# Kernel tuning notes

Measured on AMD Instinct MI355X. Metric: run time of the kernel, lower is better.

## Reference

```python
import jax, jax.numpy as jnp
import numpy as np

H_D, W_D = 64, 64          # 1024x1024 image / 16 patch size
N = H_D * W_D              # 4096 patches
D = 768                    # DINO ViT-B/16 embed dim
ALPHA = 0.5
K = 100


def setup_inputs() -> dict:
    key = jax.random.key(0)
    k1, k2 = jax.random.split(key)
    out = jax.random.normal(k1, (N, D), dtype=jnp.float32)
    attn_seed = jax.random.randint(k2, (2,), 0, H_D, dtype=jnp.int32)
    return {"out": out, "attn_seed": attn_seed}


def _connected_components(mask):
    """8-connectivity connected components via iterative min-label propagation.
    Background = 0. Foreground pixels get the minimum initial id (+1) of their
    component (same partition as cv2.connectedComponents, different numbering)."""
    fg = mask > 0
    BIG = jnp.int32(N + 1)
    init = jnp.where(fg, jnp.arange(N, dtype=jnp.int32).reshape(H_D, W_D) + 1, BIG)

    def step(l):
        p = jnp.pad(l, 1, constant_values=N + 1)
        m = l
        for dy in (0, 1, 2):          # fixed 3x3 neighborhood, not a data-dim loop
            for dx in (0, 1, 2):
                m = jnp.minimum(m, p[dy:dy + H_D, dx:dx + W_D])
        return jnp.where(fg, m, BIG)

    def cond(st):
        l, prev = st
        return jnp.any(l != prev)

    def body(st):
        l, _ = st
        return step(l), l

    l, _ = jax.lax.while_loop(cond, body, (step(init), init))
    return jnp.where(fg, l, 0)


def reference(out, attn_seed):
    # similarity between all patch features: [N, N]
    sim = out @ out.T
    deg = sim >= 0                                        # degree_matrix (bool)
    # patch with fewest non-negative similarities
    seed_degree_flat = jnp.argmin(deg.sum(axis=0)).astype(jnp.int32)
    seed_degree = jnp.stack([seed_degree_flat // W_D, seed_degree_flat % W_D])
    # blend degree seed with attention seed
    seed_rc = jnp.round(ALPHA * seed_degree + (1.0 - ALPHA) * attn_seed).astype(jnp.int32)
    seed = seed_rc[0] * W_D + seed_rc[1]

    # initial expansion set = patches positively correlated with the seed
    s = deg[seed].astype(jnp.int32)
    s = s.at[seed].set(1)                                 # degree_matrix[seed][seed] = 255 (truthy)
    order = jnp.argsort(-sim[seed])                       # descending
    s = s.at[order[K:]].set(0)                            # keep top-k most similar

    # sequential seed expansion (updates feed into later iterations)
    def step(s, i):
        grows = jnp.sum(sim[i] * (s == 1)) > 0
        s = s.at[i].set(jnp.where(s[i] == 0, 0, jnp.where(grows, 1, 0)))
        return s, None

    s, _ = jax.lax.scan(step, s, jnp.arange(N))

    return _connected_components(s.reshape(H_D, W_D))
```

## Files before the change

kernel.cpp:

```cpp
#include <hip/hip_runtime.h>
#include <cstdint>

#define NP   4096
#define DD   768
#define HD   64
#define WD   64
#define KTOP 100

typedef short bf16x8 __attribute__((ext_vector_type(8)));
typedef float f32x4  __attribute__((ext_vector_type(4)));

__device__ __forceinline__ void gload_lds16(const void* g, void* l) {
    __builtin_amdgcn_global_load_lds(
        (const __attribute__((address_space(1))) unsigned int*)(uintptr_t)g,
        (__attribute__((address_space(3))) unsigned int*)(unsigned int)(uintptr_t)l,
        16, 0, 0);
}

__device__ __forceinline__ unsigned short f2bf_rne(float x) {
    unsigned b = __float_as_uint(x);
    unsigned r = b + 0x7FFFu + ((b >> 16) & 1u);
    return (unsigned short)(r >> 16);
}
__device__ __forceinline__ float bf2f(unsigned short h) {
    return __uint_as_float(((unsigned)h) << 16);
}

__global__ __launch_bounds__(256) void k_split(const float* __restrict__ A,
                                               unsigned short* __restrict__ hi,
                                               unsigned short* __restrict__ lo,
                                               int* __restrict__ counts) {
    if (blockIdx.x < 16) counts[blockIdx.x * 256 + threadIdx.x] = 0;
    int idx = blockIdx.x * 256 + threadIdx.x;
    float4 v = ((const float4*)A)[idx];
    unsigned short h0 = f2bf_rne(v.x), h1 = f2bf_rne(v.y),
                   h2 = f2bf_rne(v.z), h3 = f2bf_rne(v.w);
    unsigned short l0 = f2bf_rne(v.x - bf2f(h0)), l1 = f2bf_rne(v.y - bf2f(h1)),
                   l2 = f2bf_rne(v.z - bf2f(h2)), l3 = f2bf_rne(v.w - bf2f(h3));
    ((ushort4*)hi)[idx] = make_ushort4(h0, h1, h2, h3);
    ((ushort4*)lo)[idx] = make_ushort4(l0, l1, l2, l3);
}

template<int BCH>
__device__ __forceinline__ void stage_groupN(const unsigned short* __restrict__ hi,
                                             const unsigned short* __restrict__ lo,
                                             int i0, int j0, int kbase, int tid,
                                             unsigned short* G) {
#pragma unroll
    for (int q = 0; q < (1024 + BCH) / 512; ++q) {
        int pp = q * 512 + tid;
        int ppt = pp & 1023;
        int row = ppt >> 3;
        int kcl = (ppt & 7) ^ (row & 7);
        int rbase = (pp < 1024) ? i0 : j0;
        const unsigned short* src =
            ((kcl < 4) ? hi : lo) + (size_t)(rbase + row) * DD + kbase + (kcl & 3) * 8;
        gload_lds16(src, G + pp * 8);
    }
}

__global__ __launch_bounds__(512, 4) void k_gemm(const unsigned short* __restrict__ hi,
                                                 const unsigned short* __restrict__ lo,
                                                 int* __restrict__ counts) {
    __shared__ __align__(16) unsigned short G[2][2048 * 8];
    __shared__ int colc[128];
    __shared__ int rowc[128];

    int job = blockIdx.x;
    int half = (job >= 512);
    int p = half ? (512 + ((job - 512) >> 1)) : job;
    int hh = half ? ((job - 512) & 1) : 0;

    int t = ((p & 7) * 66) + (p >> 3);
    int SI = 0, SJ = 0, rem = t;
    for (;;) {
        int sz = (SI == SJ) ? 36 : 64;
        if (rem < sz) break;
        rem -= sz;
        if (++SJ == 4) { ++SI; SJ = SI; }
    }
    int li, lj;
    if (SI == SJ) {
        int r = 0;
        while (rem >= (8 - r)) { rem -= (8 - r); ++r; }
        li = r; lj = r + rem;
    } else { li = rem >> 3; lj = rem & 7; }
    int bi = SI * 8 + li, bj = SJ * 8 + lj;
    int i0 = bi * 128, j0 = bj * 128 + hh * 64;
    int offd = (bi != bj);

    int tid = threadIdx.x;
    int lane = tid & 63, w = tid >> 6;
    int wm = w & 1, wn = w >> 1;

    int kcf = lane >> 4;
    int paH[4], paL[4];
#pragma unroll
    for (int tt = 0; tt < 4; ++tt) {
        int arow = wm * 64 + tt * 16 + (lane & 15);
        paH[tt] = arow * 8 + (kcf ^ (arow & 7));
        paL[tt] = arow * 8 + ((kcf + 4) ^ (arow & 7));
    }

    f32x4 acc[4][2];
#pragma unroll
    for (int ti = 0; ti < 4; ++ti)
#pragma unroll
        for (int u = 0; u < 2; ++u) { acc[ti][u][0] = 0.f; acc[ti][u][1] = 0.f;
                                      acc[ti][u][2] = 0.f; acc[ti][u][3] = 0.f; }

    int nl = lane & 15;
    int rg = lane >> 4;

    if (!half) {
        int pbH[2], pbL[2];
#pragma unroll
        for (int u = 0; u < 2; ++u) {
            int brow = wn * 32 + u * 16 + (lane & 15);
            pbH[u] = 1024 + brow * 8 + (kcf ^ (brow & 7));
            pbL[u] = 1024 + brow * 8 + ((kcf + 4) ^ (brow & 7));
        }
        stage_groupN<1024>(hi, lo, i0, j0, 0, tid, G[0]);
        for (int it = 0; it < 24; ++it) {
            int cur = it & 1;
            __syncthreads();
            if (it + 1 < 24)
                stage_groupN<1024>(hi, lo, i0, j0, (it + 1) * 32, tid, G[cur ^ 1]);
            bf16x8 ahi[4], alo[4], bhi[2], blo[2];
#pragma unroll
            for (int tt = 0; tt < 4; ++tt) {
                ahi[tt] = *(const bf16x8*)&G[cur][paH[tt] * 8];
                alo[tt] = *(const bf16x8*)&G[cur][paL[tt] * 8];
            }
#pragma unroll
            for (int u = 0; u < 2; ++u) {
                bhi[u] = *(const bf16x8*)&G[cur][pbH[u] * 8];
                blo[u] = *(const bf16x8*)&G[cur][pbL[u] * 8];
            }
#pragma unroll
            for (int ti = 0; ti < 4; ++ti)
#pragma unroll
                for (int u = 0; u < 2; ++u) {
                    acc[ti][u] = __builtin_amdgcn_mfma_f32_16x16x32_bf16(
                        ahi[ti], bhi[u], acc[ti][u], 0, 0, 0);
                    acc[ti][u] = __builtin_amdgcn_mfma_f32_16x16x32_bf16(
                        alo[ti], bhi[u], acc[ti][u], 0, 0, 0);
                    acc[ti][u] = __builtin_amdgcn_mfma_f32_16x16x32_bf16(
                        ahi[ti], blo[u], acc[ti][u], 0, 0, 0);
                }
        }

        if (tid < 128) { colc[tid] = 0; rowc[tid] = 0; }
        __syncthreads();
        int cc[2] = {0, 0};
#pragma unroll
        for (int ti = 0; ti < 4; ++ti)
#pragma unroll
            for (int u = 0; u < 2; ++u) {
                f32x4 a = acc[ti][u];
                cc[u] += ((a[0] >= 0.f) ? 1 : 0) + ((a[1] >= 0.f) ? 1 : 0) +
                         ((a[2] >= 0.f) ? 1 : 0) + ((a[3] >= 0.f) ? 1 : 0);
            }
#pragma unroll
        for (int u = 0; u < 2; ++u) {
            int v = cc[u];
            v += __shfl_xor(v, 16);
            v += __shfl_xor(v, 32);
            if (rg == 0) atomicAdd(&colc[wn * 32 + u * 16 + nl], v);
        }
        if (offd) {
#pragma unroll
            for (int ti = 0; ti < 4; ++ti)
#pragma unroll
                for (int g = 0; g < 4; ++g) {
                    int rv = ((acc[ti][0][g] >= 0.f) ? 1 : 0) +
                             ((acc[ti][1][g] >= 0.f) ? 1 : 0);
                    rv += __shfl_xor(rv, 1);
                    rv += __shfl_xor(rv, 2);
                    rv += __shfl_xor(rv, 4);
                    rv += __shfl_xor(rv, 8);
                    if (nl == 0) atomicAdd(&rowc[wm * 64 + ti * 16 + rg * 4 + g], rv);
                }
        }
        __syncthreads();
        if (tid < 128) {
            atomicAdd(&counts[j0 + tid], colc[tid]);
            if (offd) atomicAdd(&counts[i0 + tid], rowc[tid]);
        }
    } else {
        int brow = wn * 16 + (lane & 15);
        int pbH0 = 1024 + brow * 8 + (kcf ^ (brow & 7));
        int pbL0 = 1024 + brow * 8 + ((kcf + 4) ^ (brow & 7));

        stage_groupN<512>(hi, lo, i0, j0, 0, tid, G[0]);
        for (int it = 0; it < 24; ++it) {
            int cur = it & 1;
            __syncthreads();
            if (it + 1 < 24)
                stage_groupN<512>(hi, lo, i0, j0, (it + 1) * 32, tid, G[cur ^ 1]);
            bf16x8 ahi[4], alo[4], bhi0, blo0;
#pragma unroll
            for (int tt = 0; tt < 4; ++tt) {
                ahi[tt] = *(const bf16x8*)&G[cur][paH[tt] * 8];
                alo[tt] = *(const bf16x8*)&G[cur][paL[tt] * 8];
            }
            bhi0 = *(const bf16x8*)&G[cur][pbH0 * 8];
            blo0 = *(const bf16x8*)&G[cur][pbL0 * 8];
#pragma unroll
            for (int ti = 0; ti < 4; ++ti) {
                acc[ti][0] = __builtin_amdgcn_mfma_f32_16x16x32_bf16(
                    ahi[ti], bhi0, acc[ti][0], 0, 0, 0);
                acc[ti][0] = __builtin_amdgcn_mfma_f32_16x16x32_bf16(
                    alo[ti], bhi0, acc[ti][0], 0, 0, 0);
                acc[ti][0] = __builtin_amdgcn_mfma_f32_16x16x32_bf16(
                    ahi[ti], blo0, acc[ti][0], 0, 0, 0);
            }
        }

        if (tid < 128) { colc[tid] = 0; rowc[tid] = 0; }
        __syncthreads();
        int cc0 = 0;
#pragma unroll
        for (int ti = 0; ti < 4; ++ti) {
            f32x4 a = acc[ti][0];
            cc0 += ((a[0] >= 0.f) ? 1 : 0) + ((a[1] >= 0.f) ? 1 : 0) +
                   ((a[2] >= 0.f) ? 1 : 0) + ((a[3] >= 0.f) ? 1 : 0);
        }
        {
            int v = cc0;
            v += __shfl_xor(v, 16);
            v += __shfl_xor(v, 32);
            if (rg == 0) atomicAdd(&colc[wn * 16 + nl], v);
        }
        if (offd) {
#pragma unroll
            for (int ti = 0; ti < 4; ++ti)
#pragma unroll
                for (int g = 0; g < 4; ++g) {
                    int rv = ((acc[ti][0][g] >= 0.f) ? 1 : 0);
                    rv += __shfl_xor(rv, 1);
                    rv += __shfl_xor(rv, 2);
                    rv += __shfl_xor(rv, 4);
                    rv += __shfl_xor(rv, 8);
                    if (nl == 0) atomicAdd(&rowc[wm * 64 + ti * 16 + rg * 4 + g], rv);
                }
        }
        __syncthreads();
        if (tid < 64) atomicAdd(&counts[j0 + tid], colc[tid]);
        if (tid < 128 && offd) atomicAdd(&counts[i0 + tid], rowc[tid]);
    }
}

__device__ __forceinline__ int block_sum256(int v, int lane, int w, int* wred) {
#pragma unroll
    for (int o = 1; o < 64; o <<= 1) v += __shfl_xor(v, o);
    if (lane == 0) wred[w] = v;
    __syncthreads();
    int tt = wred[0] + wred[1] + wred[2] + wred[3];
    __syncthreads();
    return tt;
}
__device__ __forceinline__ int block_exscan256(int v, int lane, int w, int* wred,
                                               int* total) {
    int inc = v;
#pragma unroll
    for (int o = 1; o < 64; o <<= 1) { int u = __shfl_up(inc, o); if (lane >= o) inc += u; }
    if (lane == 63) wred[w] = inc;
    __syncthreads();
    int w0 = wred[0], w1 = wred[1], w2 = wred[2], w3 = wred[3];
    int wofs = (w > 0 ? w0 : 0) + (w > 1 ? w1 : 0) + (w > 2 ? w2 : 0);
    *total = w0 + w1 + w2 + w3;
    __syncthreads();
    return wofs + inc - v;
}

__global__ __launch_bounds__(256) void k_seedrow(const float* __restrict__ A,
                                                 const int* __restrict__ counts,
                                                 const int* __restrict__ attn_seed,
                                                 float* __restrict__ simrow,
                                                 int* __restrict__ seedp,
                                                 int* __restrict__ outp) {
    __shared__ int redA[256], redB[256];
    int tid = threadIdx.x, lane = tid & 63, w = tid >> 6;
    int blk = blockIdx.x;

    int bc = 0x7fffffff, bI = 0;
    for (int j = tid; j < NP; j += 256) {
        int c = counts[j];
        if (c < bc) { bc = c; bI = j; }
    }
    redA[tid] = bc; redB[tid] = bI;
    __syncthreads();
    for (int st = 128; st > 0; st >>= 1) {
        if (tid < st) {
            if (redA[tid + st] < redA[tid] ||
                (redA[tid + st] == redA[tid] && redB[tid + st] < redB[tid])) {
                redA[tid] = redA[tid + st];
                redB[tid] = redB[tid + st];
            }
        }
        __syncthreads();
    }
    int flat = redB[0];
    int sr = flat / WD, sc = flat % WD;
    int vr = sr + attn_seed[0];
    int vc = sc + attn_seed[1];
    int rr, rc;
    if ((vr & 1) == 0) rr = vr >> 1;
    else { int m = vr >> 1; rr = (m & 1) ? m + 1 : m; }
    if ((vc & 1) == 0) rc = vc >> 1;
    else { int m = vc >> 1; rc = (m & 1) ? m + 1 : m; }
    int seed = rr * WD + rc;
    if (blk == 0 && tid == 0) seedp[0] = seed;

    float sv[12];
#pragma unroll
    for (int kk = 0; kk < 12; ++kk) sv[kk] = A[(size_t)seed * DD + lane + kk * 64];
    int jbase = blk * 8 + w * 2;
#pragma unroll
    for (int jj = 0; jj < 2; ++jj) {
        int j = jbase + jj;
        float sum = 0.f;
#pragma unroll
        for (int kk = 0; kk < 12; ++kk)
            sum += sv[kk] * A[(size_t)j * DD + lane + kk * 64];
#pragma unroll
        for (int o = 32; o > 0; o >>= 1) sum += __shfl_down(sum, o);
        if (lane == 0) simrow[j] = sum;
    }
    if (blk < 128 && tid < 32) outp[blk * 32 + tid] = 0;
}

__global__ __launch_bounds__(256) void k_subsel(const float* __restrict__ A,
                                                const float* __restrict__ simrow,
                                                const int* __restrict__ seedp,
                                                int* __restrict__ act, int* __restrict__ Mp,
                                                float* __restrict__ subsim) {
    __shared__ int wred[4];
    __shared__ int act_s[128];
    __shared__ float av[DD];
    int tid = threadIdx.x, lane = tid & 63, w = tid >> 6;
    int seed = seedp[0];
    int base = tid * 16;
    unsigned key[16];
#pragma unroll
    for (int n = 0; n < 16; ++n) {
        unsigned b = __float_as_uint(simrow[base + n]);
        key[n] = (b & 0x80000000u) ? ~b : (b | 0x80000000u);
    }
    unsigned prefix = 0;
    for (int bit = 31; bit >= 0; --bit) {
        unsigned cand = prefix | (1u << bit);
        int c = 0;
#pragma unroll
        for (int n = 0; n < 16; ++n) c += (key[n] >= cand) ? 1 : 0;
        int tot = block_sum256(c, lane, w, wred);
        if (tot >= KTOP) prefix = cand;
    }
    unsigned KT = prefix;
    int cgt = 0, ceq = 0;
#pragma unroll
    for (int n = 0; n < 16; ++n) {
        cgt += (key[n] > KT) ? 1 : 0;
        ceq += (key[n] == KT) ? 1 : 0;
    }
    int totgt = block_sum256(cgt, lane, w, wred);
    int slots = KTOP - totgt;
    int dummy;
    int eqrun = block_exscan256(ceq, lane, w, wred, &dummy);
    int flag[16]; int cf = 0;
#pragma unroll
    for (int n = 0; n < 16; ++n) {
        int j = base + n;
        unsigned k = key[n];
        int topk = (k > KT) || (k == KT && eqrun < slots);
        if (k == KT) ++eqrun;
        int f = (topk && (k >= 0x80000000u || j == seed)) ? 1 : 0;
        flag[n] = f; cf += f;
    }
    int M;
    int off = block_exscan256(cf, lane, w, wred, &M);
#pragma unroll
    for (int n = 0; n < 16; ++n)
        if (flag[n]) act_s[off++] = base + n;
    __syncthreads();

    int p = blockIdx.x;
    if (p == 0) {
        if (tid == 0) Mp[0] = M;
        if (tid < M) act[tid] = act_s[tid];
    }
    if (p >= M) return;

    int ip = act_s[p];
    for (int k = tid; k < DD; k += 256) av[k] = A[(size_t)ip * DD + k];
    __syncthreads();
    for (int q = w; q < M; q += 4) {
        int iq = act_s[q];
        float sum = 0.f;
#pragma unroll
        for (int kk = 0; kk < 12; ++kk) {
            int k = lane + kk * 64;
            sum += av[k] * A[(size_t)iq * DD + k];
        }
#pragma unroll
        for (int o = 32; o > 0; o >>= 1) sum += __shfl_down(sum, o);
        if (lane == 0) subsim[p * 128 + q] = sum;
    }
}

__global__ __launch_bounds__(256) void k_fin(const float* __restrict__ subsim,
                                             const int* __restrict__ act,
                                             const int* __restrict__ Mp,
                                             int* __restrict__ outp) {
    __shared__ float ss[128 * 128];
    __shared__ int act_s[128];
    __shared__ int alive[128];
    __shared__ int lab[128];
    __shared__ unsigned char nbr[128][8];
    __shared__ int ncnt[128];
    __shared__ int chg;
    int M = Mp[0];
    int tid = threadIdx.x, lane = tid & 63;

    if (tid < 128) act_s[tid] = (tid < M) ? act[tid] : 0;
    for (int i4 = tid; i4 < M * 32; i4 += 256) {
        int p = i4 >> 5, qb = (i4 & 31) << 2;
        float4 v = ((const float4*)subsim)[i4];
        ss[(qb + 0) * 128 + ((p + qb + 0) & 127)] = v.x;
        ss[(qb + 1) * 128 + ((p + qb + 1) & 127)] = v.y;
        ss[(qb + 2) * 128 + ((p + qb + 2) & 127)] = v.z;
        ss[(qb + 3) * 128 + ((p + qb + 3) & 127)] = v.w;
    }
    __syncthreads();

    if (tid < 64) {
        float S_lo = 0.f, S_hi = 0.f;
        for (int q = 0; q < M; ++q) {
            S_lo += ss[q * 128 + ((lane + q) & 127)];
            S_hi += ss[q * 128 + ((lane + 64 + q) & 127)];
        }
        float al = (lane < M) ? 1.f : 0.f;
        float ah = (lane + 64 < M) ? 1.f : 0.f;
        for (int p = 0; p < M; ++p) {
            float Sp = (p < 64) ? __shfl(S_lo, p) : __shfl(S_hi, p - 64);
            if (!(Sp > 0.f)) {
                S_lo -= ss[p * 128 + ((lane + p) & 127)];
                S_hi -= ss[p * 128 + ((lane + 64 + p) & 127)];
                if (lane == p)      al = 0.f;
                if (lane + 64 == p) ah = 0.f;
            }
        }
        alive[lane]      = (lane < M && al != 0.f) ? 1 : 0;
        alive[lane + 64] = (lane + 64 < M && ah != 0.f) ? 1 : 0;
    }
    __syncthreads();

    if (tid < 128) {
        int a = (tid < M) ? alive[tid] : 0;
        int c = 0;
        if (a) {
            int id = act_s[tid];
            int y = id >> 6, x = id & 63;
            for (int q = 0; q < M; ++q) {
                if (q == tid || !alive[q]) continue;
                int qid = act_s[q];
                int dy = (qid >> 6) - y, dx = (qid & 63) - x;
                if (dy >= -1 && dy <= 1 && dx >= -1 && dx <= 1)
                    nbr[tid][c++] = (unsigned char)q;
            }
        }
        ncnt[tid] = c;
        lab[tid] = a ? tid : 32767;
    }
    __syncthreads();
    while (true) {
        if (tid == 0) chg = 0;
        __syncthreads();
        int local = 0;
        if (tid < M && alive[tid]) {
            int m = lab[tid];
            int nc = ncnt[tid];
            for (int k = 0; k < nc; ++k) { int u = lab[nbr[tid][k]]; if (u < m) m = u; }
            { int u = lab[m]; if (u < m) m = u; }
            { int u = lab[m]; if (u < m) m = u; }
            if (m < lab[tid]) { lab[tid] = m; local = 1; }
        }
        if (local) chg = 1;
        __syncthreads();
        if (chg == 0) break;
        __syncthreads();
    }
    if (tid < M && alive[tid]) outp[act_s[tid]] = act_s[lab[tid]] + 1;
}

extern "C" void kernel_launch(void* const* d_in, const int* in_sizes, int n_in,
                              void* d_out, int out_size, void* d_ws, size_t ws_size,
                              hipStream_t stream) {
    const float* A = (const float*)d_in[0];
    const int* attn = (const int*)d_in[1];
    int* outp = (int*)d_out;

    char* ws = (char*)d_ws;
    int*            counts = (int*)(ws);
    float*          simrow = (float*)(ws + 16384);
    int*            act    = (int*)(ws + 32768);
    int*            Mp     = (int*)(ws + 33280);
    int*            seedp  = (int*)(ws + 33284);
    float*          subsim = (float*)(ws + 33792);
    unsigned short* hi     = (unsigned short*)(ws + 1048576);
    unsigned short* lo     = (unsigned short*)(ws + 1048576 + 6291456);

    k_split  <<<3072, 256, 0, stream>>>(A, hi, lo, counts);
    k_gemm   <<<544,  512, 0, stream>>>(hi, lo, counts);
    k_seedrow<<<512,  256, 0, stream>>>(A, counts, attn, simrow, seedp, outp);
    k_subsel <<<128,  256, 0, stream>>>(A, simrow, seedp, act, Mp, subsim);
    k_fin    <<<1,    256, 0, stream>>>(subsim, act, Mp, outp);
}
```

Baseline: 180.7 us.

## Split tail GEMM tiles into 64x64 quarters and speed up argmin/top-k reductions

The last 32 tile pairs of the symmetric Gram GEMM are now split into 64x64 quarter jobs instead of 128x64 halves, with diagonal blocks emitting only three quarters. This gives 574 smaller blocks and is meant to even out the tail of the launch. The argmin over counts now packs count and index into one key and reduces with wave shuffles instead of a shared-memory tree. The top-k threshold radix search resolves two bits per pass with packed 16-bit counts, halving the number of block-wide reductions, at the cost of more compares per pass.

```diff
diff --git a/kernel.cpp b/kernel.cpp
--- a/kernel.cpp
+++ b/kernel.cpp
@@ -41,13 +41,12 @@
     ((ushort4*)lo)[idx] = make_ushort4(l0, l1, l2, l3);
 }
 
-template<int BCH>
-__device__ __forceinline__ void stage_groupN(const unsigned short* __restrict__ hi,
-                                             const unsigned short* __restrict__ lo,
-                                             int i0, int j0, int kbase, int tid,
-                                             unsigned short* G) {
-#pragma unroll
-    for (int q = 0; q < (1024 + BCH) / 512; ++q) {
+__device__ __forceinline__ void stage_full(const unsigned short* __restrict__ hi,
+                                           const unsigned short* __restrict__ lo,
+                                           int i0, int j0, int kbase, int tid,
+                                           unsigned short* G) {
+#pragma unroll
+    for (int q = 0; q < 4; ++q) {
         int pp = q * 512 + tid;
         int ppt = pp & 1023;
         int row = ppt >> 3;
@@ -59,6 +58,24 @@
     }
 }
 
+__device__ __forceinline__ void stage_quarter(const unsigned short* __restrict__ hi,
+                                              const unsigned short* __restrict__ lo,
+                                              int i0, int j0, int kbase, int tid,
+                                              unsigned short* G) {
+#pragma unroll
+    for (int q = 0; q < 2; ++q) {
+        int pp = q * 512 + tid;
+        int isB = pp >= 512;
+        int ppt = pp & 511;
+        int row = ppt >> 3;
+        int kcl = (ppt & 7) ^ (row & 7);
+        int rbase = isB ? j0 : i0;
+        const unsigned short* src =
+            ((kcl < 4) ? hi : lo) + (size_t)(rbase + row) * DD + kbase + (kcl & 3) * 8;
+        gload_lds16(src, G + pp * 8);
+    }
+}
+
 __global__ __launch_bounds__(512, 4) void k_gemm(const unsigned short* __restrict__ hi,
                                                  const unsigned short* __restrict__ lo,
                                                  int* __restrict__ counts) {
@@ -67,9 +84,23 @@
     __shared__ int rowc[128];
 
     int job = blockIdx.x;
-    int half = (job >= 512);
-    int p = half ? (512 + ((job - 512) >> 1)) : job;
-    int hh = half ? ((job - 512) & 1) : 0;
+    int p, qr = 0, qc = 0;
+    if (job < 512) {
+        p = job;
+    } else {
+        int r = job - 512;
+        p = 512;
+        for (;;) {
+            int nj = (p == 523 || p == 527) ? 3 : 4;
+            if (r < nj) break;
+            r -= nj; ++p;
+        }
+        if (p == 523 || p == 527) {
+            qr = (r == 1); qc = (r >= 1);
+        } else {
+            qr = r >> 1; qc = r & 1;
+        }
+    }
 
     int t = ((p & 7) * 66) + (p >> 3);
     int SI = 0, SJ = 0, rem = t;
@@ -81,51 +112,48 @@
     }
     int li, lj;
     if (SI == SJ) {
-        int r = 0;
-        while (rem >= (8 - r)) { rem -= (8 - r); ++r; }
-        li = r; lj = r + rem;
+        int r2 = 0;
+        while (rem >= (8 - r2)) { rem -= (8 - r2); ++r2; }
+        li = r2; lj = r2 + rem;
     } else { li = rem >> 3; lj = rem & 7; }
     int bi = SI * 8 + li, bj = SJ * 8 + lj;
-    int i0 = bi * 128, j0 = bj * 128 + hh * 64;
-    int offd = (bi != bj);
 
     int tid = threadIdx.x;
     int lane = tid & 63, w = tid >> 6;
     int wm = w & 1, wn = w >> 1;
-
     int kcf = lane >> 4;
-    int paH[4], paL[4];
-#pragma unroll
-    for (int tt = 0; tt < 4; ++tt) {
-        int arow = wm * 64 + tt * 16 + (lane & 15);
-        paH[tt] = arow * 8 + (kcf ^ (arow & 7));
-        paL[tt] = arow * 8 + ((kcf + 4) ^ (arow & 7));
-    }
-
-    f32x4 acc[4][2];
-#pragma unroll
-    for (int ti = 0; ti < 4; ++ti)
-#pragma unroll
-        for (int u = 0; u < 2; ++u) { acc[ti][u][0] = 0.f; acc[ti][u][1] = 0.f;
-                                      acc[ti][u][2] = 0.f; acc[ti][u][3] = 0.f; }
-
     int nl = lane & 15;
     int rg = lane >> 4;
 
-    if (!half) {
-        int pbH[2], pbL[2];
+    if (job < 512) {
+        int i0 = bi * 128, j0 = bj * 128;
+        int offd = (bi != bj);
+        int paH[4], paL[4], pbH[2], pbL[2];
+#pragma unroll
+        for (int tt = 0; tt < 4; ++tt) {
+            int arow = wm * 64 + tt * 16 + (lane & 15);
+            paH[tt] = arow * 8 + (kcf ^ (arow & 7));
+            paL[tt] = arow * 8 + ((kcf + 4) ^ (arow & 7));
+        }
 #pragma unroll
         for (int u = 0; u < 2; ++u) {
             int brow = wn * 32 + u * 16 + (lane & 15);
             pbH[u] = 1024 + brow * 8 + (kcf ^ (brow & 7));
             pbL[u] = 1024 + brow * 8 + ((kcf + 4) ^ (brow & 7));
         }
-        stage_groupN<1024>(hi, lo, i0, j0, 0, tid, G[0]);
+        f32x4 acc[4][2];
+#pragma unroll
+        for (int ti = 0; ti < 4; ++ti)
+#pragma unroll
+            for (int u = 0; u < 2; ++u) { acc[ti][u][0] = 0.f; acc[ti][u][1] = 0.f;
+                                          acc[ti][u][2] = 0.f; acc[ti][u][3] = 0.f; }
+
+        stage_full(hi, lo, i0, j0, 0, tid, G[0]);
         for (int it = 0; it < 24; ++it) {
             int cur = it & 1;
             __syncthreads();
             if (it + 1 < 24)
-                stage_groupN<1024>(hi, lo, i0, j0, (it + 1) * 32, tid, G[cur ^ 1]);
+                stage_full(hi, lo, i0, j0, (it + 1) * 32, tid, G[cur ^ 1]);
             bf16x8 ahi[4], alo[4], bhi[2], blo[2];
 #pragma unroll
             for (int tt = 0; tt < 4; ++tt) {
@@ -188,41 +216,57 @@
             if (offd) atomicAdd(&counts[i0 + tid], rowc[tid]);
         }
     } else {
+        int i0 = bi * 128 + qr * 64, j0 = bj * 128 + qc * 64;
+        int offd = (bi != bj) || (qr != qc);
+        int paH[2], paL[2];
+#pragma unroll
+        for (int tt = 0; tt < 2; ++tt) {
+            int arow = wm * 32 + tt * 16 + (lane & 15);
+            paH[tt] = arow * 8 + (kcf ^ (arow & 7));
+            paL[tt] = arow * 8 + ((kcf + 4) ^ (arow & 7));
+        }
         int brow = wn * 16 + (lane & 15);
-        int pbH0 = 1024 + brow * 8 + (kcf ^ (brow & 7));
-        int pbL0 = 1024 + brow * 8 + ((kcf + 4) ^ (brow & 7));
-
-        stage_groupN<512>(hi, lo, i0, j0, 0, tid, G[0]);
+        int pbH0 = 512 + brow * 8 + (kcf ^ (brow & 7));
+        int pbL0 = 512 + brow * 8 + ((kcf + 4) ^ (brow & 7));
+
+        f32x4 acc[2];
+#pragma unroll
+        for (int ti = 0; ti < 2; ++ti) { acc[ti][0] = 0.f; acc[ti][1] = 0.f;
+                                         acc[ti][2] = 0.f; acc[ti][3] = 0.f; }
+
+        stage_quarter(hi, lo, i0, j0, 0, tid, G[0]);
         for (int it = 0; it < 24; ++it) {
             int cur = it & 1;
             __syncthreads();
             if (it + 1 < 24)
-                stage_groupN<512>(hi, lo, i0, j0, (it + 1) * 32, tid, G[cur ^ 1]);
-            bf16x8 ahi[4], alo[4], bhi0, blo0;
-#pragma unroll
-            for (int tt = 0; tt < 4; ++tt) {
+                stage_quarter(hi, lo, i0, j0, (it + 1) * 32, tid, G[cur ^ 1]);
+            bf16x8 ahi[2], alo[2], bhi0, blo0;
+#pragma unroll
+            for (int tt = 0; tt < 2; ++tt) {
                 ahi[tt] = *(const bf16x8*)&G[cur][paH[tt] * 8];
                 alo[tt] = *(const bf16x8*)&G[cur][paL[tt] * 8];
             }
             bhi0 = *(const bf16x8*)&G[cur][pbH0 * 8];
             blo0 = *(const bf16x8*)&G[cur][pbL0 * 8];
 #pragma unroll
-            for (int ti = 0; ti < 4; ++ti) {
-                acc[ti][0] = __builtin_amdgcn_mfma_f32_16x16x32_bf16(
-                    ahi[ti], bhi0, acc[ti][0], 0, 0, 0);
-                acc[ti][0] = __builtin_amdgcn_mfma_f32_16x16x32_bf16(
-                    alo[ti], bhi0, acc[ti][0], 0, 0, 0);
-                acc[ti][0] = __builtin_amdgcn_mfma_f32_16x16x32_bf16(
-                    ahi[ti], blo0, acc[ti][0], 0, 0, 0);
-            }
-        }
-
-        if (tid < 128) { colc[tid] = 0; rowc[tid] = 0; }
+            for (int ti = 0; ti < 2; ++ti) {
+                acc[ti] = __builtin_amdgcn_mfma_f32_16x16x32_bf16(
+                    ahi[ti], bhi0, acc[ti], 0, 0, 0);
+                acc[ti] = __builtin_amdgcn_mfma_f32_16x16x32_bf16(
+                    alo[ti], bhi0, acc[ti], 0, 0, 0);
+                acc[ti] = __builtin_amdgcn_mfma_f32_16x16x32_bf16(
+                    ahi[ti], blo0, acc[ti], 0, 0, 0);
+            }
+        }
+
+        int* colq = colc;
+        int* rowq = colc + 64;
+        if (tid < 128) colc[tid] = 0;
         __syncthreads();
         int cc0 = 0;
 #pragma unroll
-        for (int ti = 0; ti < 4; ++ti) {
-            f32x4 a = acc[ti][0];
+        for (int ti = 0; ti < 2; ++ti) {
+            f32x4 a = acc[ti];
             cc0 += ((a[0] >= 0.f) ? 1 : 0) + ((a[1] >= 0.f) ? 1 : 0) +
                    ((a[2] >= 0.f) ? 1 : 0) + ((a[3] >= 0.f) ? 1 : 0);
         }
@@ -230,24 +274,26 @@
             int v = cc0;
             v += __shfl_xor(v, 16);
             v += __shfl_xor(v, 32);
-            if (rg == 0) atomicAdd(&colc[wn * 16 + nl], v);
+            if (rg == 0) atomicAdd(&colq[wn * 16 + nl], v);
         }
         if (offd) {
 #pragma unroll
-            for (int ti = 0; ti < 4; ++ti)
+            for (int ti = 0; ti < 2; ++ti)
 #pragma unroll
                 for (int g = 0; g < 4; ++g) {
-                    int rv = ((acc[ti][0][g] >= 0.f) ? 1 : 0);
+                    int rv = ((acc[ti][g] >= 0.f) ? 1 : 0);
                     rv += __shfl_xor(rv, 1);
                     rv += __shfl_xor(rv, 2);
                     rv += __shfl_xor(rv, 4);
                     rv += __shfl_xor(rv, 8);
-                    if (nl == 0) atomicAdd(&rowc[wm * 64 + ti * 16 + rg * 4 + g], rv);
+                    if (nl == 0) atomicAdd(&rowq[wm * 32 + ti * 16 + rg * 4 + g], rv);
                 }
         }
         __syncthreads();
-        if (tid < 64) atomicAdd(&counts[j0 + tid], colc[tid]);
-        if (tid < 128 && offd) atomicAdd(&counts[i0 + tid], rowc[tid]);
+        if (tid < 64) {
+            atomicAdd(&counts[j0 + tid], colq[tid]);
+            if (offd) atomicAdd(&counts[i0 + tid], rowq[tid]);
+        }
     }
 }
 
@@ -280,28 +326,25 @@
                                                  float* __restrict__ simrow,
                                                  int* __restrict__ seedp,
                                                  int* __restrict__ outp) {
-    __shared__ int redA[256], redB[256];
+    __shared__ unsigned redw[4];
     int tid = threadIdx.x, lane = tid & 63, w = tid >> 6;
     int blk = blockIdx.x;
 
-    int bc = 0x7fffffff, bI = 0;
+    unsigned bk = 0xFFFFFFFFu;
     for (int j = tid; j < NP; j += 256) {
-        int c = counts[j];
-        if (c < bc) { bc = c; bI = j; }
-    }
-    redA[tid] = bc; redB[tid] = bI;
-    __syncthreads();
-    for (int st = 128; st > 0; st >>= 1) {
-        if (tid < st) {
-            if (redA[tid + st] < redA[tid] ||
-                (redA[tid + st] == redA[tid] && redB[tid + st] < redB[tid])) {
-                redA[tid] = redA[tid + st];
-                redB[tid] = redB[tid + st];
-            }
-        }
-        __syncthreads();
-    }
-    int flat = redB[0];
+        unsigned k2 = ((unsigned)counts[j] << 12) | (unsigned)j;
+        bk = min(bk, k2);
+    }
+#pragma unroll
+    for (int o = 1; o < 64; o <<= 1) {
+        unsigned ok = __shfl_xor(bk, o);
+        bk = min(bk, ok);
+    }
+    if (lane == 0) redw[w] = bk;
+    __syncthreads();
+    unsigned m0 = min(min(redw[0], redw[1]), min(redw[2], redw[3]));
+    int flat = (int)(m0 & 0xFFFu);
+
     int sr = flat / WD, sc = flat % WD;
     int vr = sr + attn_seed[0];
     int vc = sc + attn_seed[1];
@@ -337,6 +380,7 @@
                                                 int* __restrict__ act, int* __restrict__ Mp,
                                                 float* __restrict__ subsim) {
     __shared__ int wred[4];
+    __shared__ unsigned long long rsl[16][4];
     __shared__ int act_s[128];
     __shared__ float av[DD];
     int tid = threadIdx.x, lane = tid & 63, w = tid >> 6;
@@ -349,13 +393,36 @@
         key[n] = (b & 0x80000000u) ? ~b : (b | 0x80000000u);
     }
     unsigned prefix = 0;
-    for (int bit = 31; bit >= 0; --bit) {
-        unsigned cand = prefix | (1u << bit);
-        int c = 0;
-#pragma unroll
-        for (int n = 0; n < 16; ++n) c += (key[n] >= cand) ? 1 : 0;
-        int tot = block_sum256(c, lane, w, wred);
-        if (tot >= KTOP) prefix = cand;
+    for (int pass = 0; pass < 16; ++pass) {
+        int shift = 30 - pass * 2;
+        unsigned phi = prefix >> shift;
+        int s0 = 0, s1 = 0, s2 = 0, s3 = 0;
+#pragma unroll
+        for (int n = 0; n < 16; ++n) {
+            unsigned hv = key[n] >> shift;
+            s0 += (hv >= phi) ? 1 : 0;
+            s1 += (hv >= phi + 1) ? 1 : 0;
+            s2 += (hv >= phi + 2) ? 1 : 0;
+            s3 += (hv >= phi + 3) ? 1 : 0;
+        }
+        unsigned long long pk = (unsigned long long)(unsigned)s0 |
+                                ((unsigned long long)(unsigned)s1 << 16) |
+                                ((unsigned long long)(unsigned)s2 << 32) |
+                                ((unsigned long long)(unsigned)s3 << 48);
+#pragma unroll
+        for (int o = 1; o < 64; o <<= 1) {
+            unsigned lo2 = __shfl_xor((unsigned)pk, o);
+            unsigned hi2 = __shfl_xor((unsigned)(pk >> 32), o);
+            pk += ((unsigned long long)hi2 << 32) | lo2;
+        }
+        if (lane == 0) rsl[pass][w] = pk;
+        __syncthreads();
+        unsigned long long tot = rsl[pass][0] + rsl[pass][1] + rsl[pass][2] + rsl[pass][3];
+        int c1 = (int)((tot >> 16) & 0xFFFF);
+        int c2 = (int)((tot >> 32) & 0xFFFF);
+        int c3 = (int)((tot >> 48) & 0xFFFF);
+        int d = (c3 >= KTOP) ? 3 : (c2 >= KTOP) ? 2 : (c1 >= KTOP) ? 1 : 0;
+        prefix |= (unsigned)d << shift;
     }
     unsigned KT = prefix;
     int cgt = 0, ceq = 0;
@@ -512,7 +579,7 @@
     unsigned short* lo     = (unsigned short*)(ws + 1048576 + 6291456);
 
     k_split  <<<3072, 256, 0, stream>>>(A, hi, lo, counts);
-    k_gemm   <<<544,  512, 0, stream>>>(hi, lo, counts);
+    k_gemm   <<<574,  512, 0, stream>>>(hi, lo, counts);
     k_seedrow<<<512,  256, 0, stream>>>(A, counts, attn, simrow, seedp, outp);
     k_subsel <<<128,  256, 0, stream>>>(A, simrow, seedp, act, Mp, subsim);
     k_fin    <<<1,    256, 0, stream>>>(subsim, act, Mp, outp);
```

Result: faster. 174.9 us (-3.2%).
